# Optimization experiments

Hardware: AMD Instinct MI355X
Metric: run time of the kernel (lower is better)

Reference implementation:

```python
import jax, jax.numpy as jnp
import numpy as np

N_NODES = 100000
N_EDGES = 1700000


def _build_csr(rng, n, e):
    row = rng.integers(0, n, size=e).astype(np.int64)
    col = rng.integers(0, n, size=e).astype(np.int32)
    order = np.argsort(row, kind='stable')
    row = row[order]
    col = col[order]
    rowptr = np.searchsorted(row, np.arange(n + 1)).astype(np.int32)
    return rowptr, col


def setup_inputs() -> dict:
    key = jax.random.key(0)
    k1, k2, k3, k4 = jax.random.split(key, 4)
    rng = np.random.default_rng(0)
    rowptr, colind = _build_csr(rng, N_NODES, N_EDGES)
    F_in, H, C = 256, 128, 16
    return {
        'x': jax.random.normal(k1, (N_NODES, F_in), dtype=jnp.float32),
        'edge_weight': jax.random.uniform(k2, (N_EDGES,), dtype=jnp.float32) + 0.5,
        'W1': jax.random.normal(k3, (F_in, H), dtype=jnp.float32) * (1.0 / np.sqrt(F_in)),
        'b1': jnp.zeros((H,), dtype=jnp.float32),
        'W2': jax.random.normal(k4, (H, C), dtype=jnp.float32) * (1.0 / np.sqrt(H)),
        'b2': jnp.zeros((C,), dtype=jnp.float32),
        'rowptr': jnp.asarray(rowptr),
        'colind': jnp.asarray(colind),
    }


def _rowids_from_rowptr(rowptr, n_edges):
    # CSR rowptr -> per-nnz row index, jit-friendly
    return (jnp.searchsorted(rowptr, jnp.arange(n_edges, dtype=rowptr.dtype), side='right') - 1).astype(jnp.int32)


def reference(x, edge_weight, W1, b1, W2, b2, rowptr, colind):
    n = x.shape[0]
    e = colind.shape[0]
    row = _rowids_from_rowptr(rowptr, e)
    col = colind

    # GCN symmetric normalization: D^-1/2 A D^-1/2 (cached=True -> shared by both layers)
    deg = jax.ops.segment_sum(edge_weight, row, num_segments=n)
    dinv = jnp.where(deg > 0, jax.lax.rsqrt(deg), 0.0)
    w = dinv[row] * edge_weight * dinv[col]

    def gcn_layer(h, W, b):
        h = h @ W                                   # [n, d_out]
        # SpMM: out[r] = sum_e w[e] * h[col[e]]
        msg = w[:, None] * h[col]                   # [e, d_out] gather
        return jax.ops.segment_sum(msg, row, num_segments=n) + b

    h = jax.nn.relu(gcn_layer(x, W1, b1))
    # dropout is identity in eval mode
    out = gcn_layer(h, W2, b2)
    return jax.nn.log_softmax(out, axis=1)
```

## Files before the change

kernel.cpp:

```cpp
#include <hip/hip_runtime.h>
#include <hip/hip_bf16.h>

#define F_IN 256
#define HDIM 128
#define CDIM 16

typedef unsigned short u16;
typedef unsigned int u32;

typedef __attribute__((ext_vector_type(8))) short bf16x8;
typedef __attribute__((ext_vector_type(4))) float f32x4;

__device__ __forceinline__ float asf(u32 u) {
    float f;
    __builtin_memcpy(&f, &u, 4);
    return f;
}
__device__ __forceinline__ u16 f2bf(float f) {
    u32 u;
    __builtin_memcpy(&u, &f, 4);
    u32 r = (u + 0x7FFFu + ((u >> 16) & 1u)) >> 16;
    return (u16)r;
}
__device__ __forceinline__ u32 cvtpk(float lo, float hi) {
    u32 r;
    asm("v_cvt_pk_bf16_f32 %0, %1, %2" : "=v"(r) : "v"(lo), "v"(hi));
    return r;
}

__global__ __launch_bounds__(256) void k_pre(const float* __restrict__ ew,
                                             const int* __restrict__ rowptr,
                                             const float* __restrict__ W1,
                                             float* __restrict__ dinv,
                                             u16* __restrict__ W1T,
                                             int n, int nbd) {
    if ((int)blockIdx.x >= nbd) {
        int idx = ((int)blockIdx.x - nbd) * 256 + threadIdx.x;
        if (idx < HDIM * F_IN) {
            int f = idx >> 8;
            int k = idx & 255;
            W1T[idx] = f2bf(W1[(size_t)k * HDIM + f]);
        }
        return;
    }
    int sg = threadIdx.x >> 4;
    int sl = threadIdx.x & 15;
    int r = blockIdx.x * 16 + sg;
    if (r >= n) return;
    int s = rowptr[r], e = rowptr[r + 1];
    float acc = 0.f;
    for (int i = s + sl; i < e; i += 16) acc += ew[i];
    acc += __shfl_xor(acc, 1);
    acc += __shfl_xor(acc, 2);
    acc += __shfl_xor(acc, 4);
    acc += __shfl_xor(acc, 8);
    if (sl == 0) dinv[r] = (acc > 0.f) ? rsqrtf(acc) : 0.f;
}

__global__ __launch_bounds__(256) void k_w(const float* __restrict__ ew,
                                           const int* __restrict__ rowptr,
                                           const int* __restrict__ col,
                                           const float* __restrict__ dinv,
                                           float* __restrict__ wn, int n) {
    int sg = threadIdx.x >> 4;
    int sl = threadIdx.x & 15;
    int r = blockIdx.x * 16 + sg;
    if (r >= n) return;
    float dr = dinv[r];
    int s = rowptr[r], e = rowptr[r + 1];
    for (int i = s + sl; i < e; i += 16)
        wn[i] = dr * ew[i] * dinv[col[i]];
}

__global__ __launch_bounds__(512, 4) void k_gemm1(const float* __restrict__ x,
                                                  const u16* __restrict__ W1T,
                                                  u16* __restrict__ T1, int n) {
    __shared__ u16 Bs[HDIM * F_IN];

    int tid = threadIdx.x;
#pragma unroll
    for (int it = 0; it < 8; it++) {
        int o16 = it * 512 + tid;
        u32 o = (u32)o16 * 16;
        u32 swz = o ^ (((o >> 9) & 7u) << 4);
        uint4 v = ((const uint4*)W1T)[o16];
        *(uint4*)((char*)Bs + swz) = v;
    }
    __syncthreads();

    int wave = tid >> 6;
    int lane = tid & 63;
    int lr = lane & 15;
    int kg = lane >> 4;
    int r0 = blockIdx.x * 256 + wave * 32;
    if (r0 >= n) return;

    f32x4 acc[2][8];
#pragma unroll
    for (int rg = 0; rg < 2; rg++)
#pragma unroll
        for (int ct = 0; ct < 8; ct++) acc[rg][ct] = (f32x4){0.f, 0.f, 0.f, 0.f};

    const float* arow[2];
#pragma unroll
    for (int rg = 0; rg < 2; rg++) {
        int row = r0 + rg * 16 + lr;
        arow[rg] = x + (size_t)(row < n ? row : (n - 1)) * F_IN + kg * 8;
    }

    float4 laA[2], haA[2], laB[2], haB[2];

#define LOADA(L_, H_, kkv_) do { \
        _Pragma("unroll") \
        for (int rg = 0; rg < 2; rg++) { \
            const float4* ap = (const float4*)(arow[rg] + (kkv_) * 32); \
            L_[rg] = ap[0]; H_[rg] = ap[1]; \
        } } while (0)

#define COMPUTE(L_, H_, kkv_) do { \
        bf16x8 afrag[2]; \
        _Pragma("unroll") \
        for (int rg = 0; rg < 2; rg++) { \
            u32 qa[4]; \
            qa[0] = cvtpk(L_[rg].x, L_[rg].y); \
            qa[1] = cvtpk(L_[rg].z, L_[rg].w); \
            qa[2] = cvtpk(H_[rg].x, H_[rg].y); \
            qa[3] = cvtpk(H_[rg].z, H_[rg].w); \
            __builtin_memcpy(&afrag[rg], qa, 16); \
        } \
        _Pragma("unroll") \
        for (int ct = 0; ct < 8; ct++) { \
            u32 a = (u32)(ct * 16 + lr) * (F_IN * 2) + (u32)kg * 16 + (u32)(kkv_) * 64; \
            u32 aswz = a ^ (((a >> 9) & 7u) << 4); \
            bf16x8 bfrag = *(const bf16x8*)((const char*)Bs + aswz); \
            _Pragma("unroll") \
            for (int rg = 0; rg < 2; rg++) \
                acc[rg][ct] = __builtin_amdgcn_mfma_f32_16x16x32_bf16(afrag[rg], bfrag, acc[rg][ct], 0, 0, 0); \
        } } while (0)

    LOADA(laA, haA, 0);
#pragma unroll
    for (int kk = 0; kk < 8; kk += 2) {
        LOADA(laB, haB, kk + 1);
        COMPUTE(laA, haA, kk);
        if (kk + 2 < 8) LOADA(laA, haA, kk + 2);
        COMPUTE(laB, haB, kk + 1);
    }
#undef LOADA
#undef COMPUTE

#pragma unroll
    for (int rg = 0; rg < 2; rg++) {
        int rbase = r0 + rg * 16 + kg * 4;
#pragma unroll
        for (int ct = 0; ct < 8; ct++) {
#pragma unroll
            for (int i = 0; i < 4; i += 2) {
                u32 q = cvtpk(acc[rg][ct][i], acc[rg][ct][i + 1]);
                int row0 = rbase + i;
                int row1 = rbase + i + 1;
                if (row0 < n) T1[(size_t)row0 * HDIM + ct * 16 + lr] = (u16)(q & 0xFFFFu);
                if (row1 < n) T1[(size_t)row1 * HDIM + ct * 16 + lr] = (u16)(q >> 16);
            }
        }
    }
}

__global__ __launch_bounds__(256) void k_spmm1(const u16* __restrict__ T1,
                                               const float* __restrict__ wn,
                                               const int* __restrict__ rowptr,
                                               const int* __restrict__ col,
                                               const float* __restrict__ b1,
                                               u16* __restrict__ H, int n) {
    int wave = threadIdx.x >> 6;
    int lane = threadIdx.x & 63;
    int r = blockIdx.x * 4 + wave;
    if (r >= n) return;
    int es = lane >> 4;
    int fl = lane & 15;

    int s = rowptr[r], e = rowptr[r + 1];
    int deg = e - s;
    int nwin = deg >> 4;
    float a[8];
#pragma unroll
    for (int j = 0; j < 8; j++) a[j] = 0.f;

#define ACCUM(w_, p_) do { \
        a[0] += (w_) * asf((p_).x << 16); a[1] += (w_) * asf((p_).x & 0xFFFF0000u); \
        a[2] += (w_) * asf((p_).y << 16); a[3] += (w_) * asf((p_).y & 0xFFFF0000u); \
        a[4] += (w_) * asf((p_).z << 16); a[5] += (w_) * asf((p_).z & 0xFFFF0000u); \
        a[6] += (w_) * asf((p_).w << 16); a[7] += (w_) * asf((p_).w & 0xFFFF0000u); \
    } while (0)

    int i = s + es;
    for (int w = 0; w < nwin; w++, i += 16) {
        float w0 = wn[i];      int c0 = col[i];
        float w1 = wn[i + 4];  int c1 = col[i + 4];
        float w2 = wn[i + 8];  int c2 = col[i + 8];
        float w3 = wn[i + 12]; int c3 = col[i + 12];
        uint4 p0 = *(const uint4*)(T1 + (size_t)c0 * HDIM + fl * 8);
        uint4 p1 = *(const uint4*)(T1 + (size_t)c1 * HDIM + fl * 8);
        uint4 p2 = *(const uint4*)(T1 + (size_t)c2 * HDIM + fl * 8);
        uint4 p3 = *(const uint4*)(T1 + (size_t)c3 * HDIM + fl * 8);
        ACCUM(w0, p0);
        ACCUM(w1, p1);
        ACCUM(w2, p2);
        ACCUM(w3, p3);
    }
    if (deg & 15) {
        int i1 = i + 4, i2 = i + 8, i3 = i + 12;
        int j0 = i  < e ? i  : (e - 1);
        int j1 = i1 < e ? i1 : (e - 1);
        int j2 = i2 < e ? i2 : (e - 1);
        int j3 = i3 < e ? i3 : (e - 1);
        float w0 = i  < e ? wn[j0] : 0.f;
        float w1 = i1 < e ? wn[j1] : 0.f;
        float w2 = i2 < e ? wn[j2] : 0.f;
        float w3 = i3 < e ? wn[j3] : 0.f;
        int c0 = col[j0], c1 = col[j1], c2 = col[j2], c3 = col[j3];
        uint4 p0 = *(const uint4*)(T1 + (size_t)c0 * HDIM + fl * 8);
        uint4 p1 = *(const uint4*)(T1 + (size_t)c1 * HDIM + fl * 8);
        uint4 p2 = *(const uint4*)(T1 + (size_t)c2 * HDIM + fl * 8);
        uint4 p3 = *(const uint4*)(T1 + (size_t)c3 * HDIM + fl * 8);
        ACCUM(w0, p0);
        ACCUM(w1, p1);
        ACCUM(w2, p2);
        ACCUM(w3, p3);
    }
#undef ACCUM

#pragma unroll
    for (int j = 0; j < 8; j++) {
        a[j] += __shfl_xor(a[j], 16);
        a[j] += __shfl_xor(a[j], 32);
    }

    if (es == 0) {
        const float4* bb = (const float4*)(b1 + fl * 8);
        float4 blo = bb[0], bhi = bb[1];
        float v0 = a[0] + blo.x, v1 = a[1] + blo.y;
        float v2 = a[2] + blo.z, v3 = a[3] + blo.w;
        float v4 = a[4] + bhi.x, v5 = a[5] + bhi.y;
        float v6 = a[6] + bhi.z, v7 = a[7] + bhi.w;
        v0 = v0 > 0.f ? v0 : 0.f; v1 = v1 > 0.f ? v1 : 0.f;
        v2 = v2 > 0.f ? v2 : 0.f; v3 = v3 > 0.f ? v3 : 0.f;
        v4 = v4 > 0.f ? v4 : 0.f; v5 = v5 > 0.f ? v5 : 0.f;
        v6 = v6 > 0.f ? v6 : 0.f; v7 = v7 > 0.f ? v7 : 0.f;
        uint4 o;
        o.x = cvtpk(v0, v1); o.y = cvtpk(v2, v3);
        o.z = cvtpk(v4, v5); o.w = cvtpk(v6, v7);
        *(uint4*)(H + (size_t)r * HDIM + fl * 8) = o;
    }
}

__global__ __launch_bounds__(256) void k_gemm2(const u16* __restrict__ H,
                                               const float* __restrict__ W2,
                                               float* __restrict__ U, int n) {
    int rl = threadIdx.x >> 4;
    int f = threadIdx.x & 15;
    int row = blockIdx.x * 16 + rl;
    if (row >= n) return;
    const u32* hr = (const u32*)(H + (size_t)row * HDIM);
    float acc = 0.f;
    for (int k2 = 0; k2 < HDIM / 2; k2++) {
        u32 pr = hr[k2];
        float h0 = asf(pr << 16);
        float h1 = asf(pr & 0xFFFF0000u);
        acc += h0 * W2[(size_t)(k2 * 2) * CDIM + f];
        acc += h1 * W2[(size_t)(k2 * 2 + 1) * CDIM + f];
    }
    U[(size_t)row * CDIM + f] = acc;
}

__global__ __launch_bounds__(256) void k_out(const float* __restrict__ U,
                                             const float* __restrict__ wn,
                                             const int* __restrict__ rowptr,
                                             const int* __restrict__ col,
                                             const float* __restrict__ b2,
                                             float* __restrict__ out, int n) {
    int wave = threadIdx.x >> 6;
    int lane = threadIdx.x & 63;
    int r = blockIdx.x * 4 + wave;
    if (r >= n) return;
    int es = lane >> 3;
    int fl = lane & 7;
    int s = rowptr[r], e = rowptr[r + 1];
    int deg = e - s;
    int nwin = deg >> 4;
    float a0 = 0.f, a1 = 0.f;

    int i = s + es;
    for (int w = 0; w < nwin; w++, i += 16) {
        float w0 = wn[i];     int c0 = col[i];
        float w1 = wn[i + 8]; int c1 = col[i + 8];
        float2 u0 = *(const float2*)(U + (size_t)c0 * CDIM + fl * 2);
        float2 u1 = *(const float2*)(U + (size_t)c1 * CDIM + fl * 2);
        a0 += w0 * u0.x; a1 += w0 * u0.y;
        a0 += w1 * u1.x; a1 += w1 * u1.y;
    }
    if (deg & 15) {
        int i1 = i + 8;
        int j0 = i  < e ? i  : (e - 1);
        int j1 = i1 < e ? i1 : (e - 1);
        float w0 = i  < e ? wn[j0] : 0.f;
        float w1 = i1 < e ? wn[j1] : 0.f;
        int c0 = col[j0], c1 = col[j1];
        float2 u0 = *(const float2*)(U + (size_t)c0 * CDIM + fl * 2);
        float2 u1 = *(const float2*)(U + (size_t)c1 * CDIM + fl * 2);
        a0 += w0 * u0.x; a1 += w0 * u0.y;
        a0 += w1 * u1.x; a1 += w1 * u1.y;
    }

    a0 += __shfl_xor(a0, 8);  a1 += __shfl_xor(a1, 8);
    a0 += __shfl_xor(a0, 16); a1 += __shfl_xor(a1, 16);
    a0 += __shfl_xor(a0, 32); a1 += __shfl_xor(a1, 32);

    float2 bp = ((const float2*)b2)[fl];
    float v0 = a0 + bp.x;
    float v1 = a1 + bp.y;

    float m = fmaxf(v0, v1);
    m = fmaxf(m, __shfl_xor(m, 1));
    m = fmaxf(m, __shfl_xor(m, 2));
    m = fmaxf(m, __shfl_xor(m, 4));
    float ss = __expf(v0 - m) + __expf(v1 - m);
    ss += __shfl_xor(ss, 1);
    ss += __shfl_xor(ss, 2);
    ss += __shfl_xor(ss, 4);
    float ls = __logf(ss);
    if (es == 0) {
        float2 res = {v0 - m - ls, v1 - m - ls};
        *(float2*)(out + (size_t)r * CDIM + fl * 2) = res;
    }
}

extern "C" void kernel_launch(void* const* d_in, const int* in_sizes, int n_in,
                              void* d_out, int out_size, void* d_ws, size_t ws_size,
                              hipStream_t stream) {
    const float* x      = (const float*)d_in[0];
    const float* ew     = (const float*)d_in[1];
    const float* W1     = (const float*)d_in[2];
    const float* b1     = (const float*)d_in[3];
    const float* W2     = (const float*)d_in[4];
    const float* b2     = (const float*)d_in[5];
    const int*   rowptr = (const int*)d_in[6];
    const int*   colind = (const int*)d_in[7];

    int n = in_sizes[6] - 1;
    int E = in_sizes[7];

    auto align256 = [](size_t v) { return (v + 255) & ~(size_t)255; };
    char* p = (char*)d_ws;
    float* dinv = (float*)p; p += align256((size_t)n * 4);
    float* wn   = (float*)p; p += align256((size_t)E * 4);
    u16*   T1   = (u16*)p;   p += align256((size_t)n * HDIM * 2);
    u16*   H    = (u16*)p;   p += align256((size_t)n * HDIM * 2);
    float* U    = (float*)p; p += align256((size_t)n * CDIM * 4);
    u16*   W1T  = (u16*)p;   p += align256((size_t)HDIM * F_IN * 2);
    float* out  = (float*)d_out;

    int nbd = (n + 15) / 16;
    k_pre<<<nbd + 128, 256, 0, stream>>>(ew, rowptr, W1, dinv, W1T, n, nbd);
    k_w<<<(n + 15) / 16, 256, 0, stream>>>(ew, rowptr, colind, dinv, wn, n);

    k_gemm1<<<(n + 255) / 256, 512, 0, stream>>>(x, W1T, T1, n);

    k_spmm1<<<(n + 3) / 4, 256, 0, stream>>>(T1, wn, rowptr, colind, b1, H, n);
    k_gemm2<<<(n + 15) / 16, 256, 0, stream>>>(H, W2, U, n);
    k_out<<<(n + 3) / 4, 256, 0, stream>>>(U, wn, rowptr, colind, b2, out, n);
}
```

Measured before the change: 179.0 us.

## Split SpMM1 feature dimension across two blocks, eight edge slots per wave

The first-layer SpMM now splits each row's 128 features into two halves, one per block, and doubles the grid. Within a wave, lanes are regrouped as 8 edge slots by 8 feature lanes, so each gather covers 128 bytes and each lane issues two gathers per 16-edge window instead of four. The aim is more waves in flight and more edge-level parallelism to hide gather latency. In exchange, each half-block rereads rowptr, col and wn, adds one extra shuffle-reduce step, and fetches half-rows of T1, which may lower coalescing.

```diff
diff --git a/kernel.cpp b/kernel.cpp
--- a/kernel.cpp
+++ b/kernel.cpp
@@ -174,10 +174,15 @@
                                                u16* __restrict__ H, int n) {
     int wave = threadIdx.x >> 6;
     int lane = threadIdx.x & 63;
-    int r = blockIdx.x * 4 + wave;
+    int bid = blockIdx.x;
+    int half = bid & 1;
+    int r = (bid >> 1) * 4 + wave;
     if (r >= n) return;
-    int es = lane >> 4;
-    int fl = lane & 15;
+    int es = lane >> 3;
+    int fl = lane & 7;
+
+    int fo = half * 64 + fl * 8;
+    const u16* T1h = T1 + fo;
 
     int s = rowptr[r], e = rowptr[r + 1];
     int deg = e - s;
@@ -195,49 +200,36 @@
 
     int i = s + es;
     for (int w = 0; w < nwin; w++, i += 16) {
-        float w0 = wn[i];      int c0 = col[i];
-        float w1 = wn[i + 4];  int c1 = col[i + 4];
-        float w2 = wn[i + 8];  int c2 = col[i + 8];
-        float w3 = wn[i + 12]; int c3 = col[i + 12];
-        uint4 p0 = *(const uint4*)(T1 + (size_t)c0 * HDIM + fl * 8);
-        uint4 p1 = *(const uint4*)(T1 + (size_t)c1 * HDIM + fl * 8);
-        uint4 p2 = *(const uint4*)(T1 + (size_t)c2 * HDIM + fl * 8);
-        uint4 p3 = *(const uint4*)(T1 + (size_t)c3 * HDIM + fl * 8);
+        float w0 = wn[i];     int c0 = col[i];
+        float w1 = wn[i + 8]; int c1 = col[i + 8];
+        uint4 p0 = *(const uint4*)(T1h + (size_t)c0 * HDIM);
+        uint4 p1 = *(const uint4*)(T1h + (size_t)c1 * HDIM);
         ACCUM(w0, p0);
         ACCUM(w1, p1);
-        ACCUM(w2, p2);
-        ACCUM(w3, p3);
     }
     if (deg & 15) {
-        int i1 = i + 4, i2 = i + 8, i3 = i + 12;
+        int i1 = i + 8;
         int j0 = i  < e ? i  : (e - 1);
         int j1 = i1 < e ? i1 : (e - 1);
-        int j2 = i2 < e ? i2 : (e - 1);
-        int j3 = i3 < e ? i3 : (e - 1);
         float w0 = i  < e ? wn[j0] : 0.f;
         float w1 = i1 < e ? wn[j1] : 0.f;
-        float w2 = i2 < e ? wn[j2] : 0.f;
-        float w3 = i3 < e ? wn[j3] : 0.f;
-        int c0 = col[j0], c1 = col[j1], c2 = col[j2], c3 = col[j3];
-        uint4 p0 = *(const uint4*)(T1 + (size_t)c0 * HDIM + fl * 8);
-        uint4 p1 = *(const uint4*)(T1 + (size_t)c1 * HDIM + fl * 8);
-        uint4 p2 = *(const uint4*)(T1 + (size_t)c2 * HDIM + fl * 8);
-        uint4 p3 = *(const uint4*)(T1 + (size_t)c3 * HDIM + fl * 8);
+        int c0 = col[j0], c1 = col[j1];
+        uint4 p0 = *(const uint4*)(T1h + (size_t)c0 * HDIM);
+        uint4 p1 = *(const uint4*)(T1h + (size_t)c1 * HDIM);
         ACCUM(w0, p0);
         ACCUM(w1, p1);
-        ACCUM(w2, p2);
-        ACCUM(w3, p3);
     }
 #undef ACCUM
 
 #pragma unroll
     for (int j = 0; j < 8; j++) {
+        a[j] += __shfl_xor(a[j], 8);
         a[j] += __shfl_xor(a[j], 16);
         a[j] += __shfl_xor(a[j], 32);
     }
 
     if (es == 0) {
-        const float4* bb = (const float4*)(b1 + fl * 8);
+        const float4* bb = (const float4*)(b1 + fo);
         float4 blo = bb[0], bhi = bb[1];
         float v0 = a[0] + blo.x, v1 = a[1] + blo.y;
         float v2 = a[2] + blo.z, v3 = a[3] + blo.w;
@@ -250,7 +242,7 @@
         uint4 o;
         o.x = cvtpk(v0, v1); o.y = cvtpk(v2, v3);
         o.z = cvtpk(v4, v5); o.w = cvtpk(v6, v7);
-        *(uint4*)(H + (size_t)r * HDIM + fl * 8) = o;
+        *(uint4*)(H + (size_t)r * HDIM + fo) = o;
     }
 }
 
@@ -366,7 +358,7 @@
 
     k_gemm1<<<(n + 255) / 256, 512, 0, stream>>>(x, W1T, T1, n);
 
-    k_spmm1<<<(n + 3) / 4, 256, 0, stream>>>(T1, wn, rowptr, colind, b1, H, n);
+    k_spmm1<<<2 * ((n + 3) / 4), 256, 0, stream>>>(T1, wn, rowptr, colind, b1, H, n);
     k_gemm2<<<(n + 15) / 16, 256, 0, stream>>>(H, W2, U, n);
     k_out<<<(n + 3) / 4, 256, 0, stream>>>(U, wn, rowptr, colind, b2, out, n);
 }
```

Result: slower. 199.7 us (+11.6%).
